# Kernel optimization log

Hardware: AMD Instinct MI355X
Metric: run time of the kernel (lower is better)

## Reference

```python
import jax, jax.numpy as jnp
import numpy as np

NEIGHBOUR = 3  # matches init_kwargs['neighbour']


def _conv2d(x, w, b=None, stride=1, pad=0):
    out = jax.lax.conv_general_dilated(
        x, w, (stride, stride), [(pad, pad), (pad, pad)],
        dimension_numbers=('NCHW', 'OIHW', 'NCHW'))
    if b is not None:
        out = out + b[None, :, None, None]
    return out


def _warp(x, offset, wg_w, wg_b, conv_w):
    """Deformable bilinear warp: offsets -> 4 corner gathers -> modulate -> regroup -> strided conv."""
    k = NEIGHBOUR
    N = k * k
    B, C, H, W = x.shape
    m = jax.nn.sigmoid(_conv2d(x, wg_w, wg_b, 1, 1))          # [B,N,H,W] modulation gate
    xp = jnp.pad(x, ((0, 0), (0, 0), (1, 1), (1, 1)))         # zero pad -> [B,C,H+2,W+2]
    Hp, Wp = H + 2, W + 2
    r = jnp.arange(-(k - 1) // 2, (k - 1) // 2 + 1, dtype=x.dtype)
    pnx, pny = jnp.meshgrid(r, r, indexing='ij')              # kernel-neighbour offsets p_n
    # absolute sampling positions in padded coords (p_0 starts at 1 due to padding)
    p0x = jnp.arange(1, H + 1, dtype=x.dtype)[None, :, None, None]
    p0y = jnp.arange(1, W + 1, dtype=x.dtype)[None, None, :, None]
    off = offset.transpose(0, 2, 3, 1)                        # [B,H,W,2N]; first N = x, last N = y
    px = p0x + pnx.ravel()[None, None, None, :] + off[..., :N]  # [B,H,W,N]
    py = p0y + pny.ravel()[None, None, None, :] + off[..., N:]
    fx = jnp.floor(jax.lax.stop_gradient(px))                 # p.detach().floor()
    fy = jnp.floor(jax.lax.stop_gradient(py))
    qx_lt = jnp.clip(fx, 0, Hp - 1)
    qy_lt = jnp.clip(fy, 0, Wp - 1)
    qx_rb = jnp.clip(fx + 1, 0, Hp - 1)
    qy_rb = jnp.clip(fy + 1, 0, Wp - 1)
    px = jnp.clip(px, 0, Hp - 1)
    py = jnp.clip(py, 0, Wp - 1)
    # bilinear weights (same algebra as the torch code)
    g_lt = (1 + (qx_lt - px)) * (1 + (qy_lt - py))
    g_rb = (1 - (qx_rb - px)) * (1 - (qy_rb - py))
    g_lb = (1 + (qx_lt - px)) * (1 - (qy_rb - py))
    g_rt = (1 - (qx_rb - px)) * (1 + (qy_lt - py))
    ix_lt = qx_lt.astype(jnp.int32); iy_lt = qy_lt.astype(jnp.int32)
    ix_rb = qx_rb.astype(jnp.int32); iy_rb = qy_rb.astype(jnp.int32)
    x_flat = xp.reshape(B, C, Hp * Wp)

    def gather(ix, iy):
        idx = (ix * Wp + iy).reshape(B, 1, H * W * N)
        return jnp.take_along_axis(x_flat, idx, axis=-1).reshape(B, C, H, W, N)

    xw = (g_lt[:, None] * gather(ix_lt, iy_lt)
          + g_rb[:, None] * gather(ix_rb, iy_rb)
          + g_lb[:, None] * gather(ix_lt, iy_rb)
          + g_rt[:, None] * gather(ix_rb, iy_lt))              # [B,C,H,W,N]
    xw = xw * m.transpose(0, 2, 3, 1)[:, None]                 # modulation, broadcast over C
    # regroup [B,C,H,W,k,k] -> [B,C,H*k,W*k] (matches _reshape_x_warped ordering)
    xw = xw.reshape(B, C, H, W, k, k).transpose(0, 1, 2, 4, 3, 5).reshape(B, C, H * k, W * k)
    return _conv2d(xw, conv_w, None, stride=k, pad=0)          # grouped-back strided conv


def setup_inputs() -> dict:
    B, C, MH, H, W = 4, 64, 18, 128, 128  # MH = 2*neighbour^2
    key = jax.random.key(0)
    ks = jax.random.split(key, 12)
    f32 = jnp.float32
    s = 0.05  # weight scale to keep gates unsaturated
    return {
        'x_t': jax.random.normal(ks[0], (B, C, H, W), f32),
        'pre_offset': jax.random.normal(ks[1], (B, MH, H, W), f32),
        'mean': jax.random.normal(ks[2], (B, MH, H, W), f32),
        'upd_w': s * jax.random.normal(ks[3], (MH, C + MH, 3, 3), f32),
        'upd_b': s * jax.random.normal(ks[4], (MH,), f32),
        'rst_w': s * jax.random.normal(ks[5], (MH, C + MH, 3, 3), f32),
        'rst_b': s * jax.random.normal(ks[6], (MH,), f32),
        'out_w': s * jax.random.normal(ks[7], (MH, C + MH, 3, 3), f32),
        'out_b': s * jax.random.normal(ks[8], (MH,), f32),
        'wg_w': s * jax.random.normal(ks[9], (9, C, 3, 3), f32),
        'wg_b': s * jax.random.normal(ks[10], (9,), f32),
        'warp_conv_w': s * jax.random.normal(ks[11], (C, C, 3, 3), f32),
    }


def reference(x_t, pre_offset, mean, upd_w, upd_b, rst_w, rst_b, out_w, out_b,
              wg_w, wg_b, warp_conv_w):
    stacked = jnp.concatenate([x_t, pre_offset], axis=1)
    update_gate = jax.nn.sigmoid(_conv2d(stacked, upd_w, upd_b, 1, 1))
    reset_gate = jax.nn.sigmoid(_conv2d(stacked, rst_w, rst_b, 1, 1))
    cand = jnp.tanh(_conv2d(jnp.concatenate([x_t, pre_offset * reset_gate], axis=1), out_w, out_b, 1, 1))
    offset = pre_offset * (1 - update_gate) + cand * update_gate
    mean_new = mean + 0.5 * (pre_offset - mean)
    offset = offset + mean_new
    x_out = _warp(x_t, offset, wg_w, wg_b, warp_conv_w)
    return (x_out, offset, mean_new)
```

## Files before the change

### kernel.cpp

```cpp
#include <hip/hip_runtime.h>
#include <hip/hip_bf16.h>
#include <math.h>

#define Bn  4
#define Cc  64
#define MHc 18
#define Hh  128
#define Wd  128
#define HW  (Hh*Wd)
#define Np  9
#define HP  130
#define WP  130
#define XPE (HP*WP*Cc)
#define PPE (HP*WP*32)
#define KX  576
#define KP  288
#define KT  (KX+KP)

typedef __attribute__((ext_vector_type(8))) short short8;
typedef __attribute__((ext_vector_type(4))) float float4v;

__device__ __forceinline__ float bf2f(__hip_bfloat16 x) { return __bfloat162float(x); }
__device__ __forceinline__ __hip_bfloat16 f2bf(float x) { return __float2bfloat16(x); }
__device__ __forceinline__ float sigm(float x) { return 1.f / (1.f + expf(-x)); }
__device__ __forceinline__ float s2f(short s) {
  return __uint_as_float(((unsigned)(unsigned short)s) << 16);
}
__device__ __forceinline__ short f2bs(float x) {
  __hip_bfloat16 h = __float2bfloat16(x);
  return *reinterpret_cast<short*>(&h);
}

#define NW1 (64*KT)
#define NW2 (32*KP)
#define NW3 (Cc*Cc*Np)

__global__ __launch_bounds__(256)
void k_prep(const float* __restrict__ x, const float* __restrict__ po,
            const float* __restrict__ upd_w, const float* __restrict__ rst_w,
            const float* __restrict__ out_w, const float* __restrict__ wg_w,
            const float* __restrict__ wcw,
            __hip_bfloat16* __restrict__ xp, __hip_bfloat16* __restrict__ pp,
            __hip_bfloat16* __restrict__ rp,
            __hip_bfloat16* __restrict__ wall, __hip_bfloat16* __restrict__ w2,
            __hip_bfloat16* __restrict__ wt) {
  __shared__ float tile[128][65];
  int blk = blockIdx.x;
  int t = threadIdx.x;
  if (blk < 512) {
    int b = blk >> 7, h = blk & 127;
    int c = t >> 2;
    int wbase = (t & 3) * 32;
    const float* src = &x[(b*Cc + c)*HW + h*Wd + wbase];
    #pragma unroll
    for (int j = 0; j < 8; ++j) {
      float4v v = *reinterpret_cast<const float4v*>(src + j*4);
      tile[wbase + j*4 + 0][c] = v.x;
      tile[wbase + j*4 + 1][c] = v.y;
      tile[wbase + j*4 + 2][c] = v.z;
      tile[wbase + j*4 + 3][c] = v.w;
    }
    __syncthreads();
    #pragma unroll
    for (int j = 0; j < 4; ++j) {
      int i = t + j * 256;
      int px = i >> 3, oct = i & 7;
      short8 ov;
      #pragma unroll
      for (int e = 0; e < 8; ++e) ov[e] = f2bs(tile[px][oct*8 + e]);
      *reinterpret_cast<short8*>(
          &xp[b*XPE + ((h+1)*WP + px + 1)*Cc + oct*8]) = ov;
    }
  } else if (blk < 1024) {
    int pb = blk - 512;
    int h = pb & 127;
    int b = pb >> 7;
    int w = t & 127;
    int half = t >> 7;
    float v[9];
    #pragma unroll
    for (int j = 0; j < 9; ++j)
      v[j] = po[(b*MHc + half*9 + j)*HW + h*Wd + w];
    #pragma unroll
    for (int j = 0; j < 9; ++j)
      pp[b*PPE + ((h+1)*WP + (w+1))*32 + half*9 + j] = f2bf(v[j]);
  } else if (blk < 1420) {
    int idx = (blk - 1024) * 256 + t;
    if (idx < NW1) {
      int k  = idx % KT;
      int gr = idx / KT;
      float v = 0.f;
      if (k < KX) {
        int n = k >> 6, ci = k & 63;
        if      (gr < 18) v = upd_w[(gr*(Cc+MHc) + ci)*9 + n];
        else if (gr < 36) v = rst_w[((gr-18)*(Cc+MHc) + ci)*9 + n];
        else if (gr < 54) v = out_w[((gr-36)*(Cc+MHc) + ci)*9 + n];
        else if (gr < 63) v = wg_w[((gr-54)*Cc + ci)*9 + n];
      } else {
        int kk = k - KX;
        int n = kk >> 5, jc = kk & 31;
        if (jc < 18) {
          if      (gr < 18) v = upd_w[(gr*(Cc+MHc) + Cc + jc)*9 + n];
          else if (gr < 36) v = rst_w[((gr-18)*(Cc+MHc) + Cc + jc)*9 + n];
        }
      }
      wall[idx] = f2bf(v);
    } else if (idx < NW1 + NW2) {
      int i2 = idx - NW1;
      int k  = i2 % KP;
      int oc = i2 / KP;
      int n = k >> 5, jc = k & 31;
      float v = (oc < 18 && jc < 18) ? out_w[(oc*(Cc+MHc) + Cc + jc)*9 + n] : 0.f;
      w2[i2] = f2bf(v);
    } else if (idx < NW1 + NW2 + NW3) {
      int i3 = idx - NW1 - NW2;
      int k  = i3 % 576;
      int co = i3 / 576;
      wt[i3] = f2bf(wcw[(co*Cc + (k & 63))*9 + (k >> 6)]);
    }
  } else {
    int bid = blk - 1420;
    int kind = bid >> 2;
    int b = bid & 3;
    short8 z = {0,0,0,0,0,0,0,0};
    if (kind == 0) {
      __hip_bfloat16* base = xp + b*XPE;
      for (int i = t; i < 4128; i += 256) {
        int off;
        if (i < 2080) {
          int row = (i < 1040) ? 0 : 129;
          int j = (i < 1040) ? i : i - 1040;
          off = row*130*64 + j*8;
        } else {
          int i2 = i - 2080;
          int strip = i2 >> 3;
          int r = 1 + (strip & 127);
          int side = strip >> 7;
          off = (r*130 + side*129)*64 + (i2 & 7)*8;
        }
        *reinterpret_cast<short8*>(base + off) = z;
      }
    } else {
      __hip_bfloat16* base = (kind == 1 ? pp : rp) + b*PPE;
      for (int i = t; i < 2064; i += 256) {
        int off;
        if (i < 1040) {
          int row = (i < 520) ? 0 : 129;
          int j = (i < 520) ? i : i - 520;
          off = row*130*32 + j*8;
        } else {
          int i2 = i - 1040;
          int strip = i2 >> 2;
          int r = 1 + (strip & 127);
          int side = strip >> 7;
          off = (r*130 + side*129)*32 + (i2 & 3)*8;
        }
        *reinterpret_cast<short8*>(base + off) = z;
      }
    }
  }
}

__global__ __launch_bounds__(256)
void k_gates(const __hip_bfloat16* __restrict__ xpad,
             const __hip_bfloat16* __restrict__ popad,
             const __hip_bfloat16* __restrict__ wall,
             const float* __restrict__ po,
             const float* __restrict__ upd_b,
             const float* __restrict__ rst_b,
             const float* __restrict__ out_b,
             const float* __restrict__ wg_b,
             float* __restrict__ u_out,
             float* __restrict__ cx_out,
             __hip_bfloat16* __restrict__ ropad,
             __hip_bfloat16* __restrict__ m_t) {
  __shared__ __align__(16) char winx[17408];
  __shared__ __align__(16) char winp[8704];
  __shared__ __align__(16) __hip_bfloat16 roL[64][32];
  int blk = blockIdx.x;
  int wtile = blk & 3;
  int hp = (blk >> 2) & 63;
  int b = blk >> 8;
  int h0 = hp * 2;
  int w0 = wtile * 32;
  int lane = threadIdx.x & 63;
  int wave = threadIdx.x >> 6;
  int t = threadIdx.x;

  #pragma unroll
  for (int j = 0; j < 4; ++j)
    ((unsigned int*)roL)[t + j*256] = 0u;

  const __hip_bfloat16* xpb = xpad + b * XPE;
  const __hip_bfloat16* ppb = popad + b * PPE;

  for (int i = t; i < 1088; i += 256) {
    int r = i / 272, cidx = i - r * 272;
    short8 v = *reinterpret_cast<const short8*>(
        xpb + ((h0 + r) * WP + w0) * Cc + cidx * 8);
    int o = i * 16;
    *reinterpret_cast<short8*>(winx + (o ^ (((o >> 7) & 7) << 4))) = v;
  }
  for (int i = t; i < 544; i += 256) {
    int r = i / 136, cidx = i - r * 136;
    short8 v = *reinterpret_cast<const short8*>(
        ppb + ((h0 + r) * WP + w0) * 32 + cidx * 8);
    int o = i * 16;
    *reinterpret_cast<short8*>(winp + (o ^ (((o >> 6) & 3) << 4))) = v;
  }
  __syncthreads();

  int mrow = lane & 15;
  int quad = lane >> 4;
  int cotile = wave * 16;
  float4v ac[4];
  #pragma unroll
  for (int g = 0; g < 4; ++g) ac[g] = (float4v){0.f,0.f,0.f,0.f};

  #pragma unroll
  for (int ks = 0; ks < KT/32; ++ks) {
    short8 a = *reinterpret_cast<const short8*>(
        wall + (cotile + mrow) * KT + ks * 32 + quad * 8);
    if (ks < 18) {
      int n = ks >> 1;
      #pragma unroll
      for (int g = 0; g < 4; ++g) {
        int hh = g >> 1, pgi = g & 1;
        int rowidx = (n / 3 + hh) * 34 + pgi*16 + mrow + (n % 3);
        int lin = rowidx * 128 + (ks & 1) * 64 + quad * 16;
        short8 bf = *reinterpret_cast<const short8*>(
            winx + (lin ^ ((rowidx & 7) << 4)));
        ac[g] = __builtin_amdgcn_mfma_f32_16x16x32_bf16(a, bf, ac[g], 0, 0, 0);
      }
    } else {
      int n = ks - 18;
      #pragma unroll
      for (int g = 0; g < 4; ++g) {
        int hh = g >> 1, pgi = g & 1;
        int rowidx = (n / 3 + hh) * 34 + pgi*16 + mrow + (n % 3);
        int lin = rowidx * 64 + quad * 16;
        short8 bf = *reinterpret_cast<const short8*>(
            winp + (lin ^ ((rowidx & 3) << 4)));
        ac[g] = __builtin_amdgcn_mfma_f32_16x16x32_bf16(a, bf, ac[g], 0, 0, 0);
      }
    }
  }

  float pvv[4][4];
  #pragma unroll
  for (int g = 0; g < 4; ++g) {
    int hh = g >> 1, pgi = g & 1;
    int sp = (h0 + hh) * Wd + w0 + pgi*16 + mrow;
    #pragma unroll
    for (int r = 0; r < 4; ++r) {
      int gr = cotile + quad * 4 + r;
      if (gr >= 18 && gr < 36)
        pvv[g][r] = po[(b*MHc + (gr-18))*HW + sp];
    }
  }
  #pragma unroll
  for (int g = 0; g < 4; ++g) {
    int hh = g >> 1, pgi = g & 1;
    int sp = (h0 + hh) * Wd + w0 + pgi*16 + mrow;
    #pragma unroll
    for (int r = 0; r < 4; ++r) {
      int gr = cotile + quad * 4 + r;
      float v = ac[g][r];
      if (gr < 18) {
        u_out[(b*MHc + gr)*HW + sp] = sigm(v + upd_b[gr]);
      } else if (gr < 36) {
        int oc = gr - 18;
        roL[hh*32 + pgi*16 + mrow][oc] = f2bf(sigm(v + rst_b[oc]) * pvv[g][r]);
      } else if (gr < 54) {
        int oc = gr - 36;
        cx_out[(b*MHc + oc)*HW + sp] = v + out_b[oc];
      } else if (gr < 63) {
        int nn = gr - 54;
        m_t[nn*(Bn*HW) + b*HW + sp] = f2bf(sigm(v + wg_b[nn]));
      }
    }
  }
  __syncthreads();
  #pragma unroll
  for (int hh = 0; hh < 2; ++hh) {
    unsigned int* dst = (unsigned int*)(ropad + b*PPE + ((h0+1+hh)*WP + (w0+1))*32);
    #pragma unroll
    for (int k = 0; k < 2; ++k)
      dst[t + k*256] = ((unsigned int*)roL)[hh*512 + t + k*256];
  }
}

__global__ __launch_bounds__(512, 6)
void k_fuse(const __hip_bfloat16* __restrict__ xpad,
            const __hip_bfloat16* __restrict__ ropad,
            const __hip_bfloat16* __restrict__ w2,
            const __hip_bfloat16* __restrict__ wt,
            const __hip_bfloat16* __restrict__ m_t,
            const float* __restrict__ po,
            const float* __restrict__ mean,
            float* __restrict__ out_off,
            float* __restrict__ out_mn,
            float* __restrict__ out_x) {
  __shared__ __align__(16) __hip_bfloat16 xw[32][584];
  __shared__ float offL[32][18];
  __shared__ float mL[32][9];
  __shared__ __align__(16) float gw[288][4];
  __shared__ __align__(16) int   ga[288][2];

  int blk = blockIdx.x;
  int wtile = blk & 3;
  int h = (blk >> 2) & 127;
  int b = blk >> 9;
  int w0 = wtile * 32;
  int lane = threadIdx.x & 63;
  int wv = threadIdx.x >> 6;
  int t = threadIdx.x;
  int mrow = lane & 15;
  int quad = lane >> 4;

  float ov[4], uv[4], pv[4], mv[4];
  int gil[4];
  int am = wv & 1, pg = wv >> 1;
  if (wv < 4) {
    int sp = h * Wd + w0 + pg*16 + mrow;
    #pragma unroll
    for (int r = 0; r < 4; ++r) {
      int gr = am*16 + quad * 4 + r;
      gil[r] = (b*MHc + gr)*HW + sp;
      if (gr < 18) {
        ov[r] = out_off[gil[r]];
        uv[r] = out_mn[gil[r]];
        pv[r] = po[gil[r]];
        mv[r] = mean[gil[r]];
      }
    }
  }
  if (t < 288) {
    int n = t >> 5, px = t & 31;
    mL[px][n] = bf2f(m_t[n*(Bn*HW) + b*HW + h*Wd + w0 + px]);
  }

  if (wv < 4) {
    const __hip_bfloat16* rpb = ropad + b * PPE;
    float4v acc = {0.f, 0.f, 0.f, 0.f};
    #pragma unroll
    for (int ks = 0; ks < 9; ++ks) {
      short8 a = *reinterpret_cast<const short8*>(
          w2 + (am*16 + mrow) * KP + ks * 32 + quad * 8);
      short8 bfr = *reinterpret_cast<const short8*>(
          rpb + ((h + ks/3) * WP + w0 + pg*16 + mrow + ks%3) * 32 + quad * 8);
      acc = __builtin_amdgcn_mfma_f32_16x16x32_bf16(a, bfr, acc, 0, 0, 0);
    }
    #pragma unroll
    for (int r = 0; r < 4; ++r) {
      int gr = am*16 + quad * 4 + r;
      if (gr < 18) {
        float cand = tanhf(ov[r] + acc[r]);
        float mn = 0.5f * (mv[r] + pv[r]);
        float off = pv[r] * (1.f - uv[r]) + cand * uv[r] + mn;
        out_off[gil[r]] = off;
        out_mn[gil[r]]  = mn;
        offL[pg*16 + mrow][gr] = off;
      }
    }
  }
  __syncthreads();

  if (t < 288) {
    int px = t / 9;
    int n = t - px * 9;
    int wp = w0 + px;
    float ox = offL[px][n];
    float oy = offL[px][9 + n];
    float mnv = mL[px][n];
    float px_ = (float)(h + 1) + (float)(n / 3 - 1) + ox;
    float py_ = (float)(wp + 1) + (float)(n % 3 - 1) + oy;
    float fx = floorf(px_), fy = floorf(py_);
    float xlt = fminf(fmaxf(fx,       0.f), 129.f);
    float ylt = fminf(fmaxf(fy,       0.f), 129.f);
    float xrb = fminf(fmaxf(fx + 1.f, 0.f), 129.f);
    float yrb = fminf(fmaxf(fy + 1.f, 0.f), 129.f);
    float pxc = fminf(fmaxf(px_, 0.f), 129.f);
    float pyc = fminf(fmaxf(py_, 0.f), 129.f);
    float glt = (1.f + xlt - pxc) * (1.f + ylt - pyc);
    float grb = (1.f - xrb + pxc) * (1.f - yrb + pyc);
    float glb = (1.f + xlt - pxc) * (1.f - yrb + pyc);
    float grt = (1.f - xrb + pxc) * (1.f + ylt - pyc);
    int ixl = (int)xlt, iyl = (int)ylt, ixr = (int)xrb, iyr = (int)yrb;
    bool yAdj = (iyr == iyl + 1);
    gw[t][0] = (glt + (yAdj ? 0.f : glb)) * mnv;
    gw[t][1] = (yAdj ? glb : 0.f) * mnv;
    gw[t][2] = (grt + (yAdj ? 0.f : grb)) * mnv;
    gw[t][3] = (yAdj ? grb : 0.f) * mnv;
    ga[t][0] = (ixl * WP + iyl) * Cc;
    ga[t][1] = (ixr * WP + iyl) * Cc;
  }
  __syncthreads();

  const __hip_bfloat16* xpb = xpad + b * XPE;
  #pragma unroll
  for (int rep = 0; rep < 2; ++rep) {
    int it = t + rep * 512;
    int qi = it >> 3, c0 = (it & 7) * 8;
    int px = qi >> 2, n = qi & 3;
    int q = px * 9 + n;
    float4v g = *reinterpret_cast<const float4v*>(gw[q]);
    int bL = ga[q][0] + c0, bR = ga[q][1] + c0;
    short8 l0 = *reinterpret_cast<const short8*>(xpb + bL);
    short8 l1 = *reinterpret_cast<const short8*>(xpb + bL + 64);
    short8 r0 = *reinterpret_cast<const short8*>(xpb + bR);
    short8 r1 = *reinterpret_cast<const short8*>(xpb + bR + 64);
    short8 ovv;
    #pragma unroll
    for (int j = 0; j < 8; ++j) {
      float vv = g.x * s2f(l0[j]);
      vv = fmaf(g.y, s2f(l1[j]), vv);
      vv = fmaf(g.z, s2f(r0[j]), vv);
      vv = fmaf(g.w, s2f(r1[j]), vv);
      ovv[j] = f2bs(vv);
    }
    *reinterpret_cast<short8*>(&xw[px][n * 64 + c0]) = ovv;
  }
  __syncthreads();

  int ct = wv & 3, pg5 = wv >> 2;
  const __hip_bfloat16* wtw = wt + (ct*16 + mrow) * 576;
  int xrow = pg5*16 + mrow;
  float4v acc = {0.f, 0.f, 0.f, 0.f};

  int qi0 = t >> 3, c00 = (t & 7) * 8;
  int px0 = qi0 / 5, n0 = 4 + (qi0 - px0 * 5);
  int q0 = px0 * 9 + n0;
  float4v g0 = *reinterpret_cast<const float4v*>(gw[q0]);
  int bL0 = ga[q0][0] + c00, bR0 = ga[q0][1] + c00;
  short8 A00 = *reinterpret_cast<const short8*>(xpb + bL0);
  short8 A10 = *reinterpret_cast<const short8*>(xpb + bL0 + 64);
  short8 A20 = *reinterpret_cast<const short8*>(xpb + bR0);
  short8 A30 = *reinterpret_cast<const short8*>(xpb + bR0 + 64);

  #pragma unroll
  for (int ks = 0; ks < 4; ++ks) {
    short8 a = *reinterpret_cast<const short8*>(wtw + ks * 32 + quad * 8);
    short8 bfr = *reinterpret_cast<const short8*>(&xw[xrow][ks * 32 + quad * 8]);
    acc = __builtin_amdgcn_mfma_f32_16x16x32_bf16(a, bfr, acc, 0, 0, 0);
  }

  {
    short8 ovv;
    #pragma unroll
    for (int j = 0; j < 8; ++j) {
      float vv = g0.x * s2f(A00[j]);
      vv = fmaf(g0.y, s2f(A10[j]), vv);
      vv = fmaf(g0.z, s2f(A20[j]), vv);
      vv = fmaf(g0.w, s2f(A30[j]), vv);
      ovv[j] = f2bs(vv);
    }
    *reinterpret_cast<short8*>(&xw[px0][n0 * 64 + c00]) = ovv;
  }
  int it1 = t + 512;
  int qi1 = it1 >> 3, c01 = (it1 & 7) * 8;
  int px1 = qi1 / 5, n1 = 4 + (qi1 - px1 * 5);
  int q1 = px1 * 9 + n1;
  float4v g1 = *reinterpret_cast<const float4v*>(gw[q1]);
  int bL1 = ga[q1][0] + c01, bR1 = ga[q1][1] + c01;
  short8 A01 = *reinterpret_cast<const short8*>(xpb + bL1);
  short8 A11 = *reinterpret_cast<const short8*>(xpb + bL1 + 64);
  short8 A21 = *reinterpret_cast<const short8*>(xpb + bR1);
  short8 A31 = *reinterpret_cast<const short8*>(xpb + bR1 + 64);

  #pragma unroll
  for (int ks = 4; ks < 6; ++ks) {
    short8 a = *reinterpret_cast<const short8*>(wtw + ks * 32 + quad * 8);
    short8 bfr = *reinterpret_cast<const short8*>(&xw[xrow][ks * 32 + quad * 8]);
    acc = __builtin_amdgcn_mfma_f32_16x16x32_bf16(a, bfr, acc, 0, 0, 0);
  }

  {
    short8 ovv;
    #pragma unroll
    for (int j = 0; j < 8; ++j) {
      float vv = g1.x * s2f(A01[j]);
      vv = fmaf(g1.y, s2f(A11[j]), vv);
      vv = fmaf(g1.z, s2f(A21[j]), vv);
      vv = fmaf(g1.w, s2f(A31[j]), vv);
      ovv[j] = f2bs(vv);
    }
    *reinterpret_cast<short8*>(&xw[px1][n1 * 64 + c01]) = ovv;
  }
  bool ok2 = (t < 256);
  int it2 = t + 1024;
  int qi2 = it2 >> 3, c02 = (it2 & 7) * 8;
  int px2 = qi2 / 5, n2 = 4 + (qi2 - px2 * 5);
  int q2 = px2 * 9 + n2;
  float4v g2 = {0.f,0.f,0.f,0.f};
  short8 A02, A12, A22, A32;
  if (ok2) {
    g2 = *reinterpret_cast<const float4v*>(gw[q2]);
    int bL2 = ga[q2][0] + c02, bR2 = ga[q2][1] + c02;
    A02 = *reinterpret_cast<const short8*>(xpb + bL2);
    A12 = *reinterpret_cast<const short8*>(xpb + bL2 + 64);
    A22 = *reinterpret_cast<const short8*>(xpb + bR2);
    A32 = *reinterpret_cast<const short8*>(xpb + bR2 + 64);
  }

  #pragma unroll
  for (int ks = 6; ks < 8; ++ks) {
    short8 a = *reinterpret_cast<const short8*>(wtw + ks * 32 + quad * 8);
    short8 bfr = *reinterpret_cast<const short8*>(&xw[xrow][ks * 32 + quad * 8]);
    acc = __builtin_amdgcn_mfma_f32_16x16x32_bf16(a, bfr, acc, 0, 0, 0);
  }

  if (ok2) {
    short8 ovv;
    #pragma unroll
    for (int j = 0; j < 8; ++j) {
      float vv = g2.x * s2f(A02[j]);
      vv = fmaf(g2.y, s2f(A12[j]), vv);
      vv = fmaf(g2.z, s2f(A22[j]), vv);
      vv = fmaf(g2.w, s2f(A32[j]), vv);
      ovv[j] = f2bs(vv);
    }
    *reinterpret_cast<short8*>(&xw[px2][n2 * 64 + c02]) = ovv;
  }
  __syncthreads();

  #pragma unroll
  for (int ks = 8; ks < 18; ++ks) {
    short8 a = *reinterpret_cast<const short8*>(wtw + ks * 32 + quad * 8);
    short8 bfr = *reinterpret_cast<const short8*>(&xw[xrow][ks * 32 + quad * 8]);
    acc = __builtin_amdgcn_mfma_f32_16x16x32_bf16(a, bfr, acc, 0, 0, 0);
  }
  #pragma unroll
  for (int r = 0; r < 4; ++r) {
    int co = ct*16 + quad * 4 + r;
    out_x[((b * Cc + co) * Hh + h) * Wd + w0 + pg5*16 + mrow] = acc[r];
  }
}

__global__ void f_convAB(const float* __restrict__ x, const float* __restrict__ po,
                         const float* __restrict__ wA, const float* __restrict__ bA,
                         const float* __restrict__ wB, const float* __restrict__ bB,
                         float* __restrict__ u_scr, float* __restrict__ ro_scr) {
  int idx = blockIdx.x * 256 + threadIdx.x;
  if (idx >= Bn * MHc * HW) return;
  int w = idx & 127, h = (idx >> 7) & 127, oc = (idx >> 14) % MHc, b = idx / (MHc*HW);
  float accA = bA[oc], accB = bB[oc];
  const float* xb = x + b*Cc*HW; const float* pb = po + b*MHc*HW;
  for (int ic = 0; ic < Cc + MHc; ++ic) {
    const float* src = (ic < Cc) ? (xb + ic*HW) : (pb + (ic-Cc)*HW);
    const float* wa = wA + (oc*(Cc+MHc)+ic)*9; const float* wb = wB + (oc*(Cc+MHc)+ic)*9;
    for (int kh = 0; kh < 3; ++kh) { int hh = h+kh-1; if ((unsigned)hh >= Hh) continue;
      for (int kw = 0; kw < 3; ++kw) { int ww = w+kw-1; if ((unsigned)ww >= Wd) continue;
        float v = src[hh*Wd+ww]; accA += v*wa[kh*3+kw]; accB += v*wb[kh*3+kw]; } }
  }
  u_scr[idx] = sigm(accA); ro_scr[idx] = sigm(accB) * pb[oc*HW + h*Wd + w];
}
__global__ void f_convC(const float* __restrict__ x, const float* __restrict__ po,
                        const float* __restrict__ mean, const float* __restrict__ wC,
                        const float* __restrict__ bC, const float* __restrict__ u_scr,
                        const float* __restrict__ ro_scr, float* __restrict__ out_off,
                        float* __restrict__ out_mean) {
  int idx = blockIdx.x * 256 + threadIdx.x;
  if (idx >= Bn * MHc * HW) return;
  int w = idx & 127, h = (idx >> 7) & 127, oc = (idx >> 14) % MHc, b = idx / (MHc*HW);
  float acc = bC[oc];
  const float* xb = x + b*Cc*HW; const float* rb = ro_scr + b*MHc*HW;
  for (int ic = 0; ic < Cc + MHc; ++ic) {
    const float* src = (ic < Cc) ? (xb + ic*HW) : (rb + (ic-Cc)*HW);
    const float* wv = wC + (oc*(Cc+MHc)+ic)*9;
    for (int kh = 0; kh < 3; ++kh) { int hh = h+kh-1; if ((unsigned)hh >= Hh) continue;
      for (int kw = 0; kw < 3; ++kw) { int ww = w+kw-1; if ((unsigned)ww >= Wd) continue;
        acc += src[hh*Wd+ww]*wv[kh*3+kw]; } }
  }
  float cand = tanhf(acc); float u = u_scr[idx]; float p = po[idx];
  float mn = 0.5f*(mean[idx]+p);
  out_off[idx] = p*(1.f-u)+cand*u+mn; out_mean[idx] = mn;
}
__global__ __launch_bounds__(256)
void f_warp(const float* __restrict__ x, const float* __restrict__ off_f,
            const float* __restrict__ wg, const float* __restrict__ bg,
            const float* __restrict__ wc, float* __restrict__ out) {
  __shared__ float mred[4][Np][64]; __shared__ float mval[4][Np];
  __shared__ float xwv[4][Np][64];
  int lane = threadIdx.x & 63, wave = threadIdx.x >> 6;
  int p = blockIdx.x * 4 + wave;
  int b = p >> 14, rem = p & 16383, h = rem >> 7, w = rem & 127;
  const float* xc = x + (b*Cc + lane)*HW;
  float part[Np];
  for (int n = 0; n < Np; ++n) part[n] = 0.f;
  for (int kh = 0; kh < 3; ++kh) { int hh = h+kh-1; if ((unsigned)hh >= Hh) continue;
    for (int kw = 0; kw < 3; ++kw) { int ww = w+kw-1; if ((unsigned)ww >= Wd) continue;
      float v = xc[hh*Wd+ww];
      for (int n = 0; n < Np; ++n) part[n] += v*wg[(n*Cc+lane)*9+kh*3+kw]; } }
  for (int n = 0; n < Np; ++n) mred[wave][n][lane] = part[n];
  __syncthreads();
  if (lane < Np) { float s = bg[lane];
    for (int c = 0; c < Cc; ++c) s += mred[wave][lane][c];
    mval[wave][lane] = sigm(s); }
  __syncthreads();
  const float* offb = off_f + b*MHc*HW; int sp = h*Wd + w;
  for (int n = 0; n < Np; ++n) {
    float px = (float)(h+1) + (float)(n/3-1) + offb[n*HW+sp];
    float py = (float)(w+1) + (float)(n%3-1) + offb[(9+n)*HW+sp];
    float fxq = floorf(px), fyq = floorf(py);
    float xlt = fminf(fmaxf(fxq,0.f),129.f), ylt = fminf(fmaxf(fyq,0.f),129.f);
    float xrb = fminf(fmaxf(fxq+1.f,0.f),129.f), yrb = fminf(fmaxf(fyq+1.f,0.f),129.f);
    float pxc = fminf(fmaxf(px,0.f),129.f), pyc = fminf(fmaxf(py,0.f),129.f);
    float glt = (1.f+xlt-pxc)*(1.f+ylt-pyc), grb = (1.f-xrb+pxc)*(1.f-yrb+pyc);
    float glb = (1.f+xlt-pxc)*(1.f-yrb+pyc), grt = (1.f-xrb+pxc)*(1.f+ylt-pyc);
    int ixl=(int)xlt, iyl=(int)ylt, ixr=(int)xrb, iyr=(int)yrb;
    float vlt=0.f,vrb=0.f,vlb=0.f,vrt=0.f;
    if (ixl>=1&&ixl<=Hh&&iyl>=1&&iyl<=Wd) vlt = xc[(ixl-1)*Wd+(iyl-1)];
    if (ixr>=1&&ixr<=Hh&&iyr>=1&&iyr<=Wd) vrb = xc[(ixr-1)*Wd+(iyr-1)];
    if (ixl>=1&&ixl<=Hh&&iyr>=1&&iyr<=Wd) vlb = xc[(ixl-1)*Wd+(iyr-1)];
    if (ixr>=1&&ixr<=Hh&&iyl>=1&&iyl<=Wd) vrt = xc[(ixr-1)*Wd+(iyl-1)];
    xwv[wave][n][lane] = (glt*vlt+grb*vrb+glb*vlb+grt*vrt)*mval[wave][n];
  }
  __syncthreads();
  float acc = 0.f;
  for (int c = 0; c < Cc; ++c)
    for (int n = 0; n < Np; ++n)
      acc += xwv[wave][n][c]*wc[(lane*Cc+c)*9+n];
  out[(b*Cc+lane)*HW + h*Wd + w] = acc;
}

extern "C" void kernel_launch(void* const* d_in, const int* in_sizes, int n_in,
                              void* d_out, int out_size, void* d_ws, size_t ws_size,
                              hipStream_t stream) {
  (void)in_sizes; (void)n_in; (void)out_size;
  const float* x_t   = (const float*)d_in[0];
  const float* po    = (const float*)d_in[1];
  const float* mean  = (const float*)d_in[2];
  const float* upd_w = (const float*)d_in[3];
  const float* upd_b = (const float*)d_in[4];
  const float* rst_w = (const float*)d_in[5];
  const float* rst_b = (const float*)d_in[6];
  const float* out_w = (const float*)d_in[7];
  const float* out_b = (const float*)d_in[8];
  const float* wg_w  = (const float*)d_in[9];
  const float* wg_b  = (const float*)d_in[10];
  const float* wcw   = (const float*)d_in[11];

  float* out_x   = (float*)d_out;
  float* out_off = out_x + 4194304;
  float* out_mn  = out_off + 1179648;

  char* ws = (char*)d_ws;
  __hip_bfloat16* xpad  = (__hip_bfloat16*)(ws + 0);
  __hip_bfloat16* popad = (__hip_bfloat16*)(ws + 8652800);
  __hip_bfloat16* ropad = (__hip_bfloat16*)(ws + 12979200);
  __hip_bfloat16* wall  = (__hip_bfloat16*)(ws + 17305600);
  __hip_bfloat16* w2    = (__hip_bfloat16*)(ws + 17416192);
  __hip_bfloat16* wt_bf = (__hip_bfloat16*)(ws + 17434624);
  __hip_bfloat16* m_t   = (__hip_bfloat16*)(ws + 17508352);
  const size_t WS_NEED = 18688000;

  if (ws_size >= WS_NEED) {
    hipLaunchKernelGGL(k_prep,  dim3(1432), dim3(256), 0, stream,
                       x_t, po, upd_w, rst_w, out_w, wg_w, wcw,
                       xpad, popad, ropad, wall, w2, wt_bf);
    hipLaunchKernelGGL(k_gates, dim3(1024), dim3(256), 0, stream,
                       xpad, popad, wall, po, upd_b, rst_b, out_b, wg_b,
                       out_mn, out_off, ropad, m_t);
    hipLaunchKernelGGL(k_fuse,  dim3(2048), dim3(512), 0, stream,
                       xpad, ropad, w2, wt_bf, m_t, po, mean,
                       out_off, out_mn, out_x);
  } else {
    float* u_scr  = out_x;
    float* cx_scr = out_x + 1179648;
    hipLaunchKernelGGL(f_convAB, dim3(4608), dim3(256), 0, stream,
                       x_t, po, upd_w, upd_b, rst_w, rst_b, u_scr, cx_scr);
    hipLaunchKernelGGL(f_convC,  dim3(4608), dim3(256), 0, stream,
                       x_t, po, mean, out_w, out_b, u_scr, cx_scr,
                       out_off, out_mn);
    hipLaunchKernelGGL(f_warp,   dim3(16384), dim3(256), 0, stream,
                       x_t, out_off, wg_w, wg_b, wcw, out_x);
  }
}
```

Baseline: 184.0 us.

## Halve k_gates tile to one row and stage popad writes through LDS

k_gates now handles one output row per block instead of two, which doubles the grid to 2048 blocks and shrinks LDS and accumulator registers. The goal is better occupancy and latency hiding at the cost of reloading more overlapping halo rows. In k_prep, the pre_offset padding pass now builds each row in shared memory, zero-fills the unused channels, and writes it out with 16-byte vector stores instead of scattered 2-byte stores.

```diff
diff --git a/kernel.cpp b/kernel.cpp
--- a/kernel.cpp
+++ b/kernel.cpp
@@ -75,6 +75,7 @@
     int pb = blk - 512;
     int h = pb & 127;
     int b = pb >> 7;
+    __hip_bfloat16* pt = (__hip_bfloat16*)&tile[0][0];
     int w = t & 127;
     int half = t >> 7;
     float v[9];
@@ -83,7 +84,20 @@
       v[j] = po[(b*MHc + half*9 + j)*HW + h*Wd + w];
     #pragma unroll
     for (int j = 0; j < 9; ++j)
-      pp[b*PPE + ((h+1)*WP + (w+1))*32 + half*9 + j] = f2bf(v[j]);
+      pt[w*32 + half*9 + j] = f2bf(v[j]);
+    for (int i = t; i < 128*14; i += 256) {
+      int px = i / 14, ch = 18 + i % 14;
+      pt[px*32 + ch] = f2bf(0.f);
+    }
+    __syncthreads();
+    #pragma unroll
+    for (int k = 0; k < 2; ++k) {
+      int i = t + k*256;
+      int px = i >> 2, oct = i & 3;
+      short8 val = *reinterpret_cast<const short8*>(pt + px*32 + oct*8);
+      *reinterpret_cast<short8*>(
+          &pp[b*PPE + ((h+1)*WP + (px+1))*32 + oct*8]) = val;
+    }
   } else if (blk < 1420) {
     int idx = (blk - 1024) * 256 + t;
     if (idx < NW1) {
@@ -174,37 +188,35 @@
              float* __restrict__ cx_out,
              __hip_bfloat16* __restrict__ ropad,
              __hip_bfloat16* __restrict__ m_t) {
-  __shared__ __align__(16) char winx[17408];
-  __shared__ __align__(16) char winp[8704];
-  __shared__ __align__(16) __hip_bfloat16 roL[64][32];
+  __shared__ __align__(16) char winx[13056];
+  __shared__ __align__(16) char winp[6528];
+  __shared__ __align__(16) __hip_bfloat16 roL[32][32];
   int blk = blockIdx.x;
   int wtile = blk & 3;
-  int hp = (blk >> 2) & 63;
-  int b = blk >> 8;
-  int h0 = hp * 2;
+  int h = (blk >> 2) & 127;
+  int b = blk >> 9;
   int w0 = wtile * 32;
   int lane = threadIdx.x & 63;
   int wave = threadIdx.x >> 6;
   int t = threadIdx.x;
 
-  #pragma unroll
-  for (int j = 0; j < 4; ++j)
-    ((unsigned int*)roL)[t + j*256] = 0u;
+  ((unsigned int*)roL)[t] = 0u;
+  ((unsigned int*)roL)[t + 256] = 0u;
 
   const __hip_bfloat16* xpb = xpad + b * XPE;
   const __hip_bfloat16* ppb = popad + b * PPE;
 
-  for (int i = t; i < 1088; i += 256) {
+  for (int i = t; i < 816; i += 256) {
     int r = i / 272, cidx = i - r * 272;
     short8 v = *reinterpret_cast<const short8*>(
-        xpb + ((h0 + r) * WP + w0) * Cc + cidx * 8);
+        xpb + ((h + r) * WP + w0) * Cc + cidx * 8);
     int o = i * 16;
     *reinterpret_cast<short8*>(winx + (o ^ (((o >> 7) & 7) << 4))) = v;
   }
-  for (int i = t; i < 544; i += 256) {
+  for (int i = t; i < 408; i += 256) {
     int r = i / 136, cidx = i - r * 136;
     short8 v = *reinterpret_cast<const short8*>(
-        ppb + ((h0 + r) * WP + w0) * 32 + cidx * 8);
+        ppb + ((h + r) * WP + w0) * 32 + cidx * 8);
     int o = i * 16;
     *reinterpret_cast<short8*>(winp + (o ^ (((o >> 6) & 3) << 4))) = v;
   }
@@ -213,81 +225,70 @@
   int mrow = lane & 15;
   int quad = lane >> 4;
   int cotile = wave * 16;
-  float4v ac[4];
-  #pragma unroll
-  for (int g = 0; g < 4; ++g) ac[g] = (float4v){0.f,0.f,0.f,0.f};
-
+  float4v acc0 = {0.f, 0.f, 0.f, 0.f};
+  float4v acc1 = {0.f, 0.f, 0.f, 0.f};
   #pragma unroll
   for (int ks = 0; ks < KT/32; ++ks) {
     short8 a = *reinterpret_cast<const short8*>(
         wall + (cotile + mrow) * KT + ks * 32 + quad * 8);
+    short8 b0, b1;
     if (ks < 18) {
       int n = ks >> 1;
-      #pragma unroll
-      for (int g = 0; g < 4; ++g) {
-        int hh = g >> 1, pgi = g & 1;
-        int rowidx = (n / 3 + hh) * 34 + pgi*16 + mrow + (n % 3);
-        int lin = rowidx * 128 + (ks & 1) * 64 + quad * 16;
-        short8 bf = *reinterpret_cast<const short8*>(
-            winx + (lin ^ ((rowidx & 7) << 4)));
-        ac[g] = __builtin_amdgcn_mfma_f32_16x16x32_bf16(a, bf, ac[g], 0, 0, 0);
-      }
+      int r0i = (n / 3) * 34 + mrow + (n % 3);
+      int r1i = r0i + 16;
+      int l0 = r0i * 128 + (ks & 1) * 64 + quad * 16;
+      int l1 = r1i * 128 + (ks & 1) * 64 + quad * 16;
+      b0 = *reinterpret_cast<const short8*>(winx + (l0 ^ ((r0i & 7) << 4)));
+      b1 = *reinterpret_cast<const short8*>(winx + (l1 ^ ((r1i & 7) << 4)));
     } else {
       int n = ks - 18;
-      #pragma unroll
-      for (int g = 0; g < 4; ++g) {
-        int hh = g >> 1, pgi = g & 1;
-        int rowidx = (n / 3 + hh) * 34 + pgi*16 + mrow + (n % 3);
-        int lin = rowidx * 64 + quad * 16;
-        short8 bf = *reinterpret_cast<const short8*>(
-            winp + (lin ^ ((rowidx & 3) << 4)));
-        ac[g] = __builtin_amdgcn_mfma_f32_16x16x32_bf16(a, bf, ac[g], 0, 0, 0);
-      }
-    }
-  }
-
-  float pvv[4][4];
-  #pragma unroll
-  for (int g = 0; g < 4; ++g) {
-    int hh = g >> 1, pgi = g & 1;
-    int sp = (h0 + hh) * Wd + w0 + pgi*16 + mrow;
-    #pragma unroll
-    for (int r = 0; r < 4; ++r) {
-      int gr = cotile + quad * 4 + r;
-      if (gr >= 18 && gr < 36)
-        pvv[g][r] = po[(b*MHc + (gr-18))*HW + sp];
-    }
-  }
-  #pragma unroll
-  for (int g = 0; g < 4; ++g) {
-    int hh = g >> 1, pgi = g & 1;
-    int sp = (h0 + hh) * Wd + w0 + pgi*16 + mrow;
-    #pragma unroll
-    for (int r = 0; r < 4; ++r) {
-      int gr = cotile + quad * 4 + r;
-      float v = ac[g][r];
-      if (gr < 18) {
-        u_out[(b*MHc + gr)*HW + sp] = sigm(v + upd_b[gr]);
-      } else if (gr < 36) {
-        int oc = gr - 18;
-        roL[hh*32 + pgi*16 + mrow][oc] = f2bf(sigm(v + rst_b[oc]) * pvv[g][r]);
-      } else if (gr < 54) {
-        int oc = gr - 36;
-        cx_out[(b*MHc + oc)*HW + sp] = v + out_b[oc];
-      } else if (gr < 63) {
-        int nn = gr - 54;
-        m_t[nn*(Bn*HW) + b*HW + sp] = f2bf(sigm(v + wg_b[nn]));
-      }
-    }
-  }
-  __syncthreads();
-  #pragma unroll
-  for (int hh = 0; hh < 2; ++hh) {
-    unsigned int* dst = (unsigned int*)(ropad + b*PPE + ((h0+1+hh)*WP + (w0+1))*32);
-    #pragma unroll
-    for (int k = 0; k < 2; ++k)
-      dst[t + k*256] = ((unsigned int*)roL)[hh*512 + t + k*256];
-  }
+      int r0i = (n / 3) * 34 + mrow + (n % 3);
+      int r1i = r0i + 16;
+      int l0 = r0i * 64 + quad * 16;
+      int l1 = r1i * 64 + quad * 16;
+      b0 = *reinterpret_cast<const short8*>(winp + (l0 ^ ((r0i & 3) << 4)));
+      b1 = *reinterpret_cast<const short8*>(winp + (l1 ^ ((r1i & 3) << 4)));
+    }
+    acc0 = __builtin_amdgcn_mfma_f32_16x16x32_bf16(a, b0, acc0, 0, 0, 0);
+    acc1 = __builtin_amdgcn_mfma_f32_16x16x32_bf16(a, b1, acc1, 0, 0, 0);
+  }
+
+  int sp0 = h * Wd + w0 + mrow;
+  int sp1 = sp0 + 16;
+  float pv0[4], pv1[4];
+  #pragma unroll
+  for (int r = 0; r < 4; ++r) {
+    int gr = cotile + quad * 4 + r;
+    if (gr >= 18 && gr < 36) {
+      pv0[r] = po[(b*MHc + (gr-18))*HW + sp0];
+      pv1[r] = po[(b*MHc + (gr-18))*HW + sp1];
+    }
+  }
+  #pragma unroll
+  for (int r = 0; r < 4; ++r) {
+    int gr = cotile + quad * 4 + r;
+    float v0 = acc0[r], v1 = acc1[r];
+    if (gr < 18) {
+      u_out[(b*MHc + gr)*HW + sp0] = sigm(v0 + upd_b[gr]);
+      u_out[(b*MHc + gr)*HW + sp1] = sigm(v1 + upd_b[gr]);
+    } else if (gr < 36) {
+      int oc = gr - 18;
+      roL[mrow][oc]      = f2bf(sigm(v0 + rst_b[oc]) * pv0[r]);
+      roL[16 + mrow][oc] = f2bf(sigm(v1 + rst_b[oc]) * pv1[r]);
+    } else if (gr < 54) {
+      int oc = gr - 36;
+      cx_out[(b*MHc + oc)*HW + sp0] = v0 + out_b[oc];
+      cx_out[(b*MHc + oc)*HW + sp1] = v1 + out_b[oc];
+    } else if (gr < 63) {
+      int nn = gr - 54;
+      m_t[nn*(Bn*HW) + b*HW + sp0] = f2bf(sigm(v0 + wg_b[nn]));
+      m_t[nn*(Bn*HW) + b*HW + sp1] = f2bf(sigm(v1 + wg_b[nn]));
+    }
+  }
+  __syncthreads();
+  unsigned int* dst = (unsigned int*)(ropad + b*PPE + ((h+1)*WP + (w0+1))*32);
+  dst[t] = ((unsigned int*)roL)[t];
+  dst[t + 256] = ((unsigned int*)roL)[t + 256];
 }
 
 __global__ __launch_bounds__(512, 6)
@@ -659,7 +660,7 @@
     hipLaunchKernelGGL(k_prep,  dim3(1432), dim3(256), 0, stream,
                        x_t, po, upd_w, rst_w, out_w, wg_w, wcw,
                        xpad, popad, ropad, wall, w2, wt_bf);
-    hipLaunchKernelGGL(k_gates, dim3(1024), dim3(256), 0, stream,
+    hipLaunchKernelGGL(k_gates, dim3(2048), dim3(256), 0, stream,
                        xpad, popad, wall, po, upd_b, rst_b, out_b, wg_b,
                        out_mn, out_off, ropad, m_t);
     hipLaunchKernelGGL(k_fuse,  dim3(2048), dim3(512), 0, stream,
```

Measured after the change: 176.4 us. 1.04x faster.
